# Kernel tuning notes

Hardware: AMD Instinct MI355X
Metric: run time of the kernel (lower is better)

The kernel has to match this reference:

```python
import jax, jax.numpy as jnp
import numpy as np

NUM_HEADS = 16
MAX_SEQ_LEN = 4096

def _rope_tables(head_dim, seq_len, dtype):
    inv_freq = 1.0 / (10000.0 ** (jnp.arange(0, head_dim, 2, dtype=jnp.float32) / head_dim))
    pos = jnp.arange(seq_len, dtype=jnp.float32)
    freqs = pos[:, None] * inv_freq[None, :]  # [S, hd/2]
    return jnp.cos(freqs).astype(dtype), jnp.sin(freqs).astype(dtype)

def _apply_rope(x, cos, sin):
    # x: [B, S, H, hd], interleaved even/odd pairs
    B, S, H, hd = x.shape
    xr = x.reshape(B, S, H, hd // 2, 2)
    xe, xo = xr[..., 0], xr[..., 1]
    c = cos[None, :, None, :]
    s = sin[None, :, None, :]
    ye = xe * c - xo * s
    yo = xe * s + xo * c
    return jnp.stack((ye, yo), axis=-1).reshape(B, S, H, hd)

def setup_inputs() -> dict:
    key = jax.random.key(0)
    k1, k2, k3 = jax.random.split(key, 3)
    B, S, D = 2, 2048, 2048
    x = jax.random.normal(k1, (B, S, D), dtype=jnp.float32)
    Wqkv = jax.random.normal(k2, (D, 3 * D), dtype=jnp.float32) * (D ** -0.5)
    Wo = jax.random.normal(k3, (D, D), dtype=jnp.float32) * (D ** -0.5)
    return {"x": x, "Wqkv": Wqkv, "Wo": Wo}

def reference(x, Wqkv, Wo):
    B, S, D = x.shape
    H = NUM_HEADS
    hd = D // H
    qkv = jnp.einsum('bsd,de->bse', x, Wqkv)  # [B,S,3D]
    q, k, v = jnp.split(qkv, 3, axis=-1)
    q = q.reshape(B, S, H, hd)
    k = k.reshape(B, S, H, hd)
    v = v.reshape(B, S, H, hd)
    cos, sin = _rope_tables(hd, S, x.dtype)
    q = _apply_rope(q, cos, sin)
    k = _apply_rope(k, cos, sin)
    scale = 1.0 / jnp.sqrt(jnp.asarray(hd, dtype=x.dtype))
    scores = jnp.einsum('bqhd,bkhd->bhqk', q, k) * scale  # [B,H,S,S]
    causal = jnp.tril(jnp.ones((S, S), dtype=bool))
    scores = jnp.where(causal[None, None], scores, jnp.asarray(-jnp.inf, dtype=scores.dtype))
    probs = jax.nn.softmax(scores, axis=-1)
    attn = jnp.einsum('bhqk,bkhd->bqhd', probs, v).reshape(B, S, D)
    return jnp.einsum('bsd,de->bse', attn, Wo)
```

## Files before the change

kernel.cpp:

```cpp
#include <hip/hip_runtime.h>
#include <cstddef>
#include <cstdint>
#include <math.h>

#define NB 2
#define NS 2048
#define ND 2048
#define NH 16
#define HD 128

typedef __attribute__((ext_vector_type(8))) short short8v;
typedef __attribute__((ext_vector_type(4))) float float4v;

#define MFMA16(A, B, C) __builtin_amdgcn_mfma_f32_16x16x32_bf16(A, B, C, 0, 0, 0)

__device__ __forceinline__ void split_bf16(float x, short& hi, short& lo) {
  unsigned u = __float_as_uint(x);
  unsigned hb = (u + 0x7FFFu + ((u >> 16) & 1u)) >> 16;
  float hif = __uint_as_float(hb << 16);
  float r = x - hif;
  unsigned ul = __float_as_uint(r);
  hi = (short)hb;
  lo = (short)((ul + 0x7FFFu + ((ul >> 16) & 1u)) >> 16);
}

__device__ __forceinline__ int pack2(short a, short b) {
  return (int)(unsigned short)a | ((int)(unsigned short)b << 16);
}

__global__ __launch_bounds__(256) void rope_table_kernel(float2* tab) {
  const int id = blockIdx.x * 256 + threadIdx.x;
  const int spos = id >> 6, p = id & 63;
  const float invf = powf(10000.f, -(float)p * (1.f / 64.f));
  float s, c;
  sincosf((float)spos * invf, &s, &c);
  tab[id] = make_float2(c, s);
}

__global__ __launch_bounds__(256) void transpose_split_kernel(
    const float* __restrict__ W, short* __restrict__ Th, short* __restrict__ Tl,
    int K, int N) {
  __shared__ float T[32][33];
  const int tid = threadIdx.x;
  const int n0 = blockIdx.x * 32, k0 = blockIdx.y * 32;
  {
    const int r = tid >> 3, c4 = (tid & 7) << 2;
    float4 v = *(const float4*)&W[(size_t)(k0 + r) * N + n0 + c4];
    T[r][c4 + 0] = v.x;
    T[r][c4 + 1] = v.y;
    T[r][c4 + 2] = v.z;
    T[r][c4 + 3] = v.w;
  }
  __syncthreads();
  const int n = tid >> 3, k4 = (tid & 7) << 2;
  short h[4], l[4];
#pragma unroll
  for (int e = 0; e < 4; ++e) split_bf16(T[k4 + e][n], h[e], l[e]);
  const size_t off = (size_t)(n0 + n) * K + k0 + k4;
  *(int2*)&Th[off] = make_int2(pack2(h[0], h[1]), pack2(h[2], h[3]));
  *(int2*)&Tl[off] = make_int2(pack2(l[0], l[1]), pack2(l[2], l[3]));
}

template <bool ROPE>
__global__ __launch_bounds__(256) void gemm_bf16x3_kernel(
    const float* __restrict__ A, const short* __restrict__ BTh,
    const short* __restrict__ BTl, float* __restrict__ C, int M, int N, int K,
    const float2* __restrict__ rope_tab) {
  __shared__ short Ah[128][40], Al[128][40];
  __shared__ short Bh[128][40], Bl[128][40];
  const int tid = threadIdx.x;
  const int wave = tid >> 6, lane = tid & 63;
  const int g = lane >> 4, r = lane & 15;
  const int wy = wave >> 1, wx = wave & 1;
  const int m0 = blockIdx.y * 128, n0 = blockIdx.x * 128;
  const int wm = wy * 64, wn = wx * 64;

  const int ar = tid >> 1, ac = (tid & 1) << 4;
  const int br = tid >> 1, bc = (tid & 1) << 4;

  const float* aptr = A + (size_t)(m0 + ar) * K + ac;
  const short* bhp = BTh + (size_t)(n0 + br) * K + bc;
  const short* blp = BTl + (size_t)(n0 + br) * K + bc;

  float4v acc[4][4];
#pragma unroll
  for (int i = 0; i < 4; ++i)
#pragma unroll
    for (int j = 0; j < 4; ++j) acc[i][j] = (float4v){0.f, 0.f, 0.f, 0.f};

  float4 a0 = *(const float4*)(aptr);
  float4 a1 = *(const float4*)(aptr + 4);
  float4 a2 = *(const float4*)(aptr + 8);
  float4 a3 = *(const float4*)(aptr + 12);
  int4 bh0 = *(const int4*)(bhp);
  int4 bh1 = *(const int4*)(bhp + 8);
  int4 bl0 = *(const int4*)(blp);
  int4 bl1 = *(const int4*)(blp + 8);

  for (int k0 = 0; k0 < K; k0 += 32) {
    __syncthreads();
    {
      float xs[16] = {a0.x, a0.y, a0.z, a0.w, a1.x, a1.y, a1.z, a1.w,
                      a2.x, a2.y, a2.z, a2.w, a3.x, a3.y, a3.z, a3.w};
      short h[16], l[16];
#pragma unroll
      for (int e = 0; e < 16; ++e) split_bf16(xs[e], h[e], l[e]);
      *(int4*)&Ah[ar][ac] =
          make_int4(pack2(h[0], h[1]), pack2(h[2], h[3]), pack2(h[4], h[5]),
                    pack2(h[6], h[7]));
      *(int4*)&Ah[ar][ac + 8] =
          make_int4(pack2(h[8], h[9]), pack2(h[10], h[11]),
                    pack2(h[12], h[13]), pack2(h[14], h[15]));
      *(int4*)&Al[ar][ac] =
          make_int4(pack2(l[0], l[1]), pack2(l[2], l[3]), pack2(l[4], l[5]),
                    pack2(l[6], l[7]));
      *(int4*)&Al[ar][ac + 8] =
          make_int4(pack2(l[8], l[9]), pack2(l[10], l[11]),
                    pack2(l[12], l[13]), pack2(l[14], l[15]));
      *(int4*)&Bh[br][bc] = bh0;
      *(int4*)&Bh[br][bc + 8] = bh1;
      *(int4*)&Bl[br][bc] = bl0;
      *(int4*)&Bl[br][bc + 8] = bl1;
    }
    __syncthreads();
    if (k0 + 32 < K) {
      const float* an = aptr + k0 + 32;
      a0 = *(const float4*)(an);
      a1 = *(const float4*)(an + 4);
      a2 = *(const float4*)(an + 8);
      a3 = *(const float4*)(an + 12);
      bh0 = *(const int4*)(bhp + k0 + 32);
      bh1 = *(const int4*)(bhp + k0 + 40);
      bl0 = *(const int4*)(blp + k0 + 32);
      bl1 = *(const int4*)(blp + k0 + 40);
    }
    short8v afh[4], afl[4], bfh[4], bfl[4];
#pragma unroll
    for (int mi = 0; mi < 4; ++mi) {
      afh[mi] = *(const short8v*)&Ah[wm + mi * 16 + r][8 * g];
      afl[mi] = *(const short8v*)&Al[wm + mi * 16 + r][8 * g];
    }
#pragma unroll
    for (int nj = 0; nj < 4; ++nj) {
      bfh[nj] = *(const short8v*)&Bh[wn + nj * 16 + r][8 * g];
      bfl[nj] = *(const short8v*)&Bl[wn + nj * 16 + r][8 * g];
    }
#pragma unroll
    for (int mi = 0; mi < 4; ++mi)
#pragma unroll
      for (int nj = 0; nj < 4; ++nj) {
        acc[mi][nj] = MFMA16(afh[mi], bfh[nj], acc[mi][nj]);
        acc[mi][nj] = MFMA16(afh[mi], bfl[nj], acc[mi][nj]);
        acc[mi][nj] = MFMA16(afl[mi], bfh[nj], acc[mi][nj]);
      }
  }

  if (ROPE && n0 < 2 * ND) {
    int p[4];
#pragma unroll
    for (int nj = 0; nj < 4; ++nj)
      p[nj] = ((n0 + wn + nj * 16 + r) & (HD - 1)) >> 1;
    const bool even = (r & 1) == 0;
#pragma unroll
    for (int mi = 0; mi < 4; ++mi)
#pragma unroll
      for (int j = 0; j < 4; ++j) {
        const int spos = (m0 + wm + mi * 16 + 4 * g + j) & (NS - 1);
#pragma unroll
        for (int nj = 0; nj < 4; ++nj) {
          const float2 cs = rope_tab[spos * 64 + p[nj]];
          const float own = acc[mi][nj][j];
          const float oth = __shfl_xor(own, 1);
          acc[mi][nj][j] = even ? own * cs.x - oth * cs.y
                                : oth * cs.y + own * cs.x;
        }
      }
  }
#pragma unroll
  for (int mi = 0; mi < 4; ++mi)
#pragma unroll
    for (int j = 0; j < 4; ++j) {
      const size_t row = m0 + wm + mi * 16 + 4 * g + j;
      float* Crow = C + row * N + n0 + wn;
#pragma unroll
      for (int nj = 0; nj < 4; ++nj) Crow[nj * 16 + r] = acc[mi][nj][j];
    }
}

template <bool ROPE>
__global__ __launch_bounds__(256) void gemm_f32_kernel(
    const float* __restrict__ A, const float* __restrict__ Bm,
    float* __restrict__ C, int M, int N, int K) {
  __shared__ float As[16][132];
  __shared__ float Bs[16][132];
  const int tid = threadIdx.x;
  const int m0 = blockIdx.y * 128;
  const int n0 = blockIdx.x * 128;
  const int tr = tid >> 4;
  const int tc = tid & 15;
  const int la_r = tid >> 1;
  const int la_c = (tid & 1) << 3;
  const int lb_r = tid >> 4;
  const int lb_c = (tid & 15) << 3;

  const float* Aptr = A + (size_t)(m0 + la_r) * K + la_c;
  const float* Bptr = Bm + (size_t)lb_r * N + n0 + lb_c;

  float acc[8][8] = {};

  float4 av0 = *(const float4*)(Aptr);
  float4 av1 = *(const float4*)(Aptr + 4);
  float4 bv0 = *(const float4*)(Bptr);
  float4 bv1 = *(const float4*)(Bptr + 4);

  for (int k0 = 0; k0 < K; k0 += 16) {
    __syncthreads();
    As[la_c + 0][la_r] = av0.x;
    As[la_c + 1][la_r] = av0.y;
    As[la_c + 2][la_r] = av0.z;
    As[la_c + 3][la_r] = av0.w;
    As[la_c + 4][la_r] = av1.x;
    As[la_c + 5][la_r] = av1.y;
    As[la_c + 6][la_r] = av1.z;
    As[la_c + 7][la_r] = av1.w;
    *(float4*)&Bs[lb_r][lb_c] = bv0;
    *(float4*)&Bs[lb_r][lb_c + 4] = bv1;
    __syncthreads();
    if (k0 + 16 < K) {
      const float* An = Aptr + k0 + 16;
      const float* Bn = Bptr + (size_t)(k0 + 16) * N;
      av0 = *(const float4*)(An);
      av1 = *(const float4*)(An + 4);
      bv0 = *(const float4*)(Bn);
      bv1 = *(const float4*)(Bn + 4);
    }
#pragma unroll
    for (int kk = 0; kk < 16; ++kk) {
      float a[8], b[8];
      *(float4*)&a[0] = *(const float4*)&As[kk][tr << 2];
      *(float4*)&a[4] = *(const float4*)&As[kk][64 + (tr << 2)];
      *(float4*)&b[0] = *(const float4*)&Bs[kk][tc << 2];
      *(float4*)&b[4] = *(const float4*)&Bs[kk][64 + (tc << 2)];
#pragma unroll
      for (int i = 0; i < 8; ++i)
#pragma unroll
        for (int j = 0; j < 8; ++j) acc[i][j] = fmaf(a[i], b[j], acc[i][j]);
    }
  }

  if (ROPE) {
    if ((n0 >> 11) < 2) {
#pragma unroll
      for (int g = 0; g < 2; ++g) {
        const int col = n0 + g * 64 + (tc << 2);
        const int d0 = col & (HD - 1);
        const int p0 = d0 >> 1;
        const float invf0 = powf(10000.f, -(float)p0 * (1.f / 64.f));
        const float invf1 = powf(10000.f, -(float)(p0 + 1) * (1.f / 64.f));
#pragma unroll
        for (int rg = 0; rg < 2; ++rg) {
#pragma unroll
          for (int i = 0; i < 4; ++i) {
            const int row = m0 + rg * 64 + (tr << 2) + i;
            const int spos = row & (NS - 1);
            float s0, c0, s1, c1;
            sincosf((float)spos * invf0, &s0, &c0);
            sincosf((float)spos * invf1, &s1, &c1);
            float* ar2 = &acc[rg * 4 + i][g * 4];
            const float xe0 = ar2[0], xo0 = ar2[1];
            const float xe1 = ar2[2], xo1 = ar2[3];
            ar2[0] = xe0 * c0 - xo0 * s0;
            ar2[1] = xe0 * s0 + xo0 * c0;
            ar2[2] = xe1 * c1 - xo1 * s1;
            ar2[3] = xe1 * s1 + xo1 * c1;
          }
        }
      }
    }
  }
#pragma unroll
  for (int rg = 0; rg < 2; ++rg) {
#pragma unroll
    for (int i = 0; i < 4; ++i) {
      const size_t row = m0 + rg * 64 + (tr << 2) + i;
      float* Crow = C + row * N + n0;
      float4 v0 = make_float4(acc[rg * 4 + i][0], acc[rg * 4 + i][1],
                              acc[rg * 4 + i][2], acc[rg * 4 + i][3]);
      float4 v1 = make_float4(acc[rg * 4 + i][4], acc[rg * 4 + i][5],
                              acc[rg * 4 + i][6], acc[rg * 4 + i][7]);
      *(float4*)(Crow + (tc << 2)) = v0;
      *(float4*)(Crow + 64 + (tc << 2)) = v1;
    }
  }
}

__global__ __launch_bounds__(512) void flash_attn_mfma(
    const float* __restrict__ qkv, float* __restrict__ O) {
  __shared__ short Khi[32][136];
  __shared__ short Klo[32][136];
  __shared__ short Vthi[128][40];
  __shared__ short Vtlo[128][40];
  __shared__ short Phi[8][16][40];
  __shared__ short Plo[8][16][40];

  const int tid = threadIdx.x;
  const int lane = tid & 63;
  const int wave = tid >> 6;
  const int g = lane >> 4;
  const int r = lane & 15;
  const int qtile = 15 - blockIdx.x;
  const int bh = blockIdx.y;
  const int b = bh >> 4, h = bh & 15;
  const int qb = qtile << 7;
  const int qw = qb + (wave << 4);
  const size_t row3d = 3 * ND;
  const float* base = qkv + (size_t)b * NS * row3d + (size_t)h * HD;
  const float* Kg = base + ND;
  const float* Vg = base + 2 * ND;

  const float scale = 0.088388347648318447f;
  const float* Qrow = base + (size_t)(qw + r) * row3d;
  short8v qhi[4], qlo[4];
#pragma unroll
  for (int hf = 0; hf < 4; ++hf) {
    const float* p = Qrow + 32 * hf + 8 * g;
    float4 x0 = *(const float4*)(p);
    float4 x1 = *(const float4*)(p + 4);
    float xs[8] = {x0.x, x0.y, x0.z, x0.w, x1.x, x1.y, x1.z, x1.w};
#pragma unroll
    for (int i = 0; i < 8; ++i) {
      short hi_, lo_;
      split_bf16(xs[i] * scale, hi_, lo_);
      qhi[hf][i] = hi_;
      qlo[hf][i] = lo_;
    }
  }

  float4v acc[8];
#pragma unroll
  for (int i = 0; i < 8; ++i) acc[i] = (float4v){0.f, 0.f, 0.f, 0.f};
  float m_run = -INFINITY;
  float l_run = 0.f;

  const int skv = tid >> 4;
  const int shd = (tid & 15) << 3;
  const int vkv = (tid & 15) << 1;
  const int vhd = (tid >> 4) << 2;
  const int ntiles = (qtile + 1) << 2;

  for (int t = 0; t < ntiles; ++t) {
    const int kvb = t << 5;
    __syncthreads();
    {
      const float* kr = Kg + (size_t)(kvb + skv) * row3d + shd;
#pragma unroll
      for (int u = 0; u < 2; ++u) {
        float4 v = *(const float4*)(kr + 4 * u);
        short h0, l0, h1, l1, h2, l2, h3, l3;
        split_bf16(v.x, h0, l0);
        split_bf16(v.y, h1, l1);
        split_bf16(v.z, h2, l2);
        split_bf16(v.w, h3, l3);
        *(int2*)&Khi[skv][shd + 4 * u] =
            make_int2(pack2(h0, h1), pack2(h2, h3));
        *(int2*)&Klo[skv][shd + 4 * u] =
            make_int2(pack2(l0, l1), pack2(l2, l3));
      }
    }
    {
      const float* v0p = Vg + (size_t)(kvb + vkv) * row3d + vhd;
      const float* v1p = v0p + row3d;
      float4 a0 = *(const float4*)(v0p);
      float4 b0 = *(const float4*)(v1p);
      float e0[4] = {a0.x, a0.y, a0.z, a0.w};
      float e1[4] = {b0.x, b0.y, b0.z, b0.w};
#pragma unroll
      for (int e = 0; e < 4; ++e) {
        short h0, l0, h1, l1;
        split_bf16(e0[e], h0, l0);
        split_bf16(e1[e], h1, l1);
        *(int*)&Vthi[vhd + e][vkv] = pack2(h0, h1);
        *(int*)&Vtlo[vhd + e][vkv] = pack2(l0, l1);
      }
    }
    __syncthreads();

    if (kvb <= qw + 15) {
      float4v s4[2];
#pragma unroll
      for (int f = 0; f < 2; ++f) s4[f] = (float4v){0.f, 0.f, 0.f, 0.f};
#pragma unroll
      for (int f = 0; f < 2; ++f) {
#pragma unroll
        for (int hf = 0; hf < 4; ++hf) {
          short8v ka = *(const short8v*)&Khi[16 * f + r][32 * hf + 8 * g];
          short8v kb = *(const short8v*)&Klo[16 * f + r][32 * hf + 8 * g];
          s4[f] = MFMA16(ka, qhi[hf], s4[f]);
          s4[f] = MFMA16(ka, qlo[hf], s4[f]);
          s4[f] = MFMA16(kb, qhi[hf], s4[f]);
        }
      }
      const int qglob = qw + r;
      if (kvb + 31 > qw) {
#pragma unroll
        for (int f = 0; f < 2; ++f)
#pragma unroll
          for (int j = 0; j < 4; ++j)
            if (kvb + 16 * f + 4 * g + j > qglob) s4[f][j] = -INFINITY;
      }
      float tmax = s4[0][0];
#pragma unroll
      for (int f = 0; f < 2; ++f)
#pragma unroll
        for (int j = 0; j < 4; ++j) tmax = fmaxf(tmax, s4[f][j]);
      tmax = fmaxf(tmax, __shfl_xor(tmax, 16));
      tmax = fmaxf(tmax, __shfl_xor(tmax, 32));
      const float mnew = fmaxf(m_run, tmax);
      const float alpha = __expf(m_run - mnew);
      float psum = 0.f;
      short ph[8], pl[8];
#pragma unroll
      for (int f = 0; f < 2; ++f)
#pragma unroll
        for (int j = 0; j < 4; ++j) {
          float p = __expf(s4[f][j] - mnew);
          psum += p;
          split_bf16(p, ph[4 * f + j], pl[4 * f + j]);
        }
      psum += __shfl_xor(psum, 16);
      psum += __shfl_xor(psum, 32);
      l_run = l_run * alpha + psum;
      m_run = mnew;
#pragma unroll
      for (int f = 0; f < 2; ++f) {
        *(int2*)&Phi[wave][r][16 * f + 4 * g] = make_int2(
            pack2(ph[4 * f + 0], ph[4 * f + 1]),
            pack2(ph[4 * f + 2], ph[4 * f + 3]));
        *(int2*)&Plo[wave][r][16 * f + 4 * g] = make_int2(
            pack2(pl[4 * f + 0], pl[4 * f + 1]),
            pack2(pl[4 * f + 2], pl[4 * f + 3]));
      }
      float aj[4];
#pragma unroll
      for (int j = 0; j < 4; ++j) aj[j] = __shfl(alpha, 4 * g + j);
#pragma unroll
      for (int hf = 0; hf < 8; ++hf)
#pragma unroll
        for (int j = 0; j < 4; ++j) acc[hf][j] *= aj[j];
      short8v pa = *(const short8v*)&Phi[wave][r][8 * g];
      short8v pb = *(const short8v*)&Plo[wave][r][8 * g];
#pragma unroll
      for (int hf = 0; hf < 8; ++hf) {
        short8v va = *(const short8v*)&Vthi[16 * hf + r][8 * g];
        short8v vb = *(const short8v*)&Vtlo[16 * hf + r][8 * g];
        acc[hf] = MFMA16(pa, va, acc[hf]);
        acc[hf] = MFMA16(pa, vb, acc[hf]);
        acc[hf] = MFMA16(pb, va, acc[hf]);
      }
    }
  }
  const float il = 1.f / l_run;
  float lj[4];
#pragma unroll
  for (int j = 0; j < 4; ++j) lj[j] = __shfl(il, 4 * g + j);
  float* Ob = O + ((size_t)b * NS + qw) * ND + h * HD;
#pragma unroll
  for (int hf = 0; hf < 8; ++hf)
#pragma unroll
    for (int j = 0; j < 4; ++j)
      Ob[(size_t)(4 * g + j) * ND + 16 * hf + r] = acc[hf][j] * lj[j];
}

extern "C" void kernel_launch(void* const* d_in, const int* in_sizes, int n_in,
                              void* d_out, int out_size, void* d_ws,
                              size_t ws_size, hipStream_t stream) {
  const float* x = (const float*)d_in[0];
  const float* Wqkv = (const float*)d_in[1];
  const float* Wo = (const float*)d_in[2];
  float* out = (float*)d_out;
  float* qkv = (float*)d_ws;
  float* attn = qkv + (size_t)NB * NS * 3 * ND;
  short* wqh = (short*)(attn + (size_t)NB * NS * ND);
  short* wql = wqh + (size_t)ND * 3 * ND;
  short* woh = wql + (size_t)ND * 3 * ND;
  short* wol = woh + (size_t)ND * ND;
  float2* tab = (float2*)(wol + (size_t)ND * ND);

  const size_t needed =
      ((size_t)NB * NS * 3 * ND + (size_t)NB * NS * ND) * 4 +
      ((size_t)ND * 3 * ND + (size_t)ND * ND) * 2 * 2 + (size_t)NS * 64 * 8;

  if (ws_size >= needed) {
    rope_table_kernel<<<NS * 64 / 256, 256, 0, stream>>>(tab);
    transpose_split_kernel<<<dim3(3 * ND / 32, ND / 32), 256, 0, stream>>>(
        Wqkv, wqh, wql, ND, 3 * ND);
    transpose_split_kernel<<<dim3(ND / 32, ND / 32), 256, 0, stream>>>(
        Wo, woh, wol, ND, ND);
    gemm_bf16x3_kernel<true>
        <<<dim3(3 * ND / 128, NB * NS / 128), 256, 0, stream>>>(
            x, wqh, wql, qkv, NB * NS, 3 * ND, ND, tab);
    flash_attn_mfma<<<dim3(16, 32), 512, 0, stream>>>(qkv, attn);
    gemm_bf16x3_kernel<false>
        <<<dim3(ND / 128, NB * NS / 128), 256, 0, stream>>>(
            attn, woh, wol, out, NB * NS, ND, ND, tab);
  } else {
    gemm_f32_kernel<true>
        <<<dim3(3 * ND / 128, NB * NS / 128), 256, 0, stream>>>(
            x, Wqkv, qkv, NB * NS, 3 * ND, ND);
    flash_attn_mfma<<<dim3(16, 32), 512, 0, stream>>>(qkv, attn);
    gemm_f32_kernel<false>
        <<<dim3(ND / 128, NB * NS / 128), 256, 0, stream>>>(
            attn, Wo, out, NB * NS, ND, ND);
  }
}
```

Before: 757.3 us.

## Pre-split activations to bf16 hi/lo and remap GEMM blocks per XCD

Adds a standalone kernel that splits x and the attention output into bf16 hi/lo arrays once. The GEMM then loads pre-split A tiles instead of redoing the split in every N-block. The GEMM also remaps block indices so each XCD works on a contiguous rectangular chunk of tiles, aiming for better L2 reuse. This costs two extra elementwise passes and more workspace, with a fallback to the old path when the workspace is too small.

```diff
diff --git a/kernel.cpp b/kernel.cpp
--- a/kernel.cpp
+++ b/kernel.cpp
@@ -35,6 +35,22 @@
   float s, c;
   sincosf((float)spos * invf, &s, &c);
   tab[id] = make_float2(c, s);
+}
+
+__global__ __launch_bounds__(256) void split_kernel(
+    const float* __restrict__ in, short* __restrict__ hi,
+    short* __restrict__ lo, int n4) {
+  for (int i = blockIdx.x * 256 + threadIdx.x; i < n4;
+       i += gridDim.x * 256) {
+    float4 v = ((const float4*)in)[i];
+    short h0, l0, h1, l1, h2, l2, h3, l3;
+    split_bf16(v.x, h0, l0);
+    split_bf16(v.y, h1, l1);
+    split_bf16(v.z, h2, l2);
+    split_bf16(v.w, h3, l3);
+    ((int2*)hi)[i] = make_int2(pack2(h0, h1), pack2(h2, h3));
+    ((int2*)lo)[i] = make_int2(pack2(l0, l1), pack2(l2, l3));
+  }
 }
 
 __global__ __launch_bounds__(256) void transpose_split_kernel(
@@ -61,9 +77,10 @@
   *(int2*)&Tl[off] = make_int2(pack2(l[0], l[1]), pack2(l[2], l[3]));
 }
 
-template <bool ROPE>
+template <bool ROPE, bool ASPLIT, int CHX, int CHY>
 __global__ __launch_bounds__(256) void gemm_bf16x3_kernel(
-    const float* __restrict__ A, const short* __restrict__ BTh,
+    const float* __restrict__ Af, const short* __restrict__ Ahg,
+    const short* __restrict__ Alg, const short* __restrict__ BTh,
     const short* __restrict__ BTl, float* __restrict__ C, int M, int N, int K,
     const float2* __restrict__ rope_tab) {
   __shared__ short Ah[128][40], Al[128][40];
@@ -72,15 +89,21 @@
   const int wave = tid >> 6, lane = tid & 63;
   const int g = lane >> 4, r = lane & 15;
   const int wy = wave >> 1, wx = wave & 1;
-  const int m0 = blockIdx.y * 128, n0 = blockIdx.x * 128;
+
+  int bx = blockIdx.x, by = blockIdx.y;
+  if (CHX > 0) {
+    const int flat = by * gridDim.x + bx;
+    const int xcd = flat & 7, idx = flat >> 3;
+    bx = (xcd & 3) * CHX + idx % CHX;
+    by = (xcd >> 2) * CHY + idx / CHX;
+  }
+  const int m0 = by * 128, n0 = bx * 128;
   const int wm = wy * 64, wn = wx * 64;
 
   const int ar = tid >> 1, ac = (tid & 1) << 4;
-  const int br = tid >> 1, bc = (tid & 1) << 4;
-
-  const float* aptr = A + (size_t)(m0 + ar) * K + ac;
-  const short* bhp = BTh + (size_t)(n0 + br) * K + bc;
-  const short* blp = BTl + (size_t)(n0 + br) * K + bc;
+
+  const short* bhp = BTh + (size_t)(n0 + ar) * K + ac;
+  const short* blp = BTl + (size_t)(n0 + ar) * K + ac;
 
   float4v acc[4][4];
 #pragma unroll
@@ -88,10 +111,25 @@
 #pragma unroll
     for (int j = 0; j < 4; ++j) acc[i][j] = (float4v){0.f, 0.f, 0.f, 0.f};
 
-  float4 a0 = *(const float4*)(aptr);
-  float4 a1 = *(const float4*)(aptr + 4);
-  float4 a2 = *(const float4*)(aptr + 8);
-  float4 a3 = *(const float4*)(aptr + 12);
+  float4 a0, a1, a2, a3;
+  int4 ah0, ah1, al0, al1;
+  const float* aptr = nullptr;
+  const short* ahp = nullptr;
+  const short* alp = nullptr;
+  if (ASPLIT) {
+    ahp = Ahg + (size_t)(m0 + ar) * K + ac;
+    alp = Alg + (size_t)(m0 + ar) * K + ac;
+    ah0 = *(const int4*)(ahp);
+    ah1 = *(const int4*)(ahp + 8);
+    al0 = *(const int4*)(alp);
+    al1 = *(const int4*)(alp + 8);
+  } else {
+    aptr = Af + (size_t)(m0 + ar) * K + ac;
+    a0 = *(const float4*)(aptr);
+    a1 = *(const float4*)(aptr + 4);
+    a2 = *(const float4*)(aptr + 8);
+    a3 = *(const float4*)(aptr + 12);
+  }
   int4 bh0 = *(const int4*)(bhp);
   int4 bh1 = *(const int4*)(bhp + 8);
   int4 bl0 = *(const int4*)(blp);
@@ -99,7 +137,12 @@
 
   for (int k0 = 0; k0 < K; k0 += 32) {
     __syncthreads();
-    {
+    if (ASPLIT) {
+      *(int4*)&Ah[ar][ac] = ah0;
+      *(int4*)&Ah[ar][ac + 8] = ah1;
+      *(int4*)&Al[ar][ac] = al0;
+      *(int4*)&Al[ar][ac + 8] = al1;
+    } else {
       float xs[16] = {a0.x, a0.y, a0.z, a0.w, a1.x, a1.y, a1.z, a1.w,
                       a2.x, a2.y, a2.z, a2.w, a3.x, a3.y, a3.z, a3.w};
       short h[16], l[16];
@@ -117,18 +160,25 @@
       *(int4*)&Al[ar][ac + 8] =
           make_int4(pack2(l[8], l[9]), pack2(l[10], l[11]),
                     pack2(l[12], l[13]), pack2(l[14], l[15]));
-      *(int4*)&Bh[br][bc] = bh0;
-      *(int4*)&Bh[br][bc + 8] = bh1;
-      *(int4*)&Bl[br][bc] = bl0;
-      *(int4*)&Bl[br][bc + 8] = bl1;
-    }
+    }
+    *(int4*)&Bh[ar][ac] = bh0;
+    *(int4*)&Bh[ar][ac + 8] = bh1;
+    *(int4*)&Bl[ar][ac] = bl0;
+    *(int4*)&Bl[ar][ac + 8] = bl1;
     __syncthreads();
     if (k0 + 32 < K) {
-      const float* an = aptr + k0 + 32;
-      a0 = *(const float4*)(an);
-      a1 = *(const float4*)(an + 4);
-      a2 = *(const float4*)(an + 8);
-      a3 = *(const float4*)(an + 12);
+      if (ASPLIT) {
+        ah0 = *(const int4*)(ahp + k0 + 32);
+        ah1 = *(const int4*)(ahp + k0 + 40);
+        al0 = *(const int4*)(alp + k0 + 32);
+        al1 = *(const int4*)(alp + k0 + 40);
+      } else {
+        const float* an = aptr + k0 + 32;
+        a0 = *(const float4*)(an);
+        a1 = *(const float4*)(an + 4);
+        a2 = *(const float4*)(an + 8);
+        a3 = *(const float4*)(an + 12);
+      }
       bh0 = *(const int4*)(bhp + k0 + 32);
       bh1 = *(const int4*)(bhp + k0 + 40);
       bl0 = *(const int4*)(blp + k0 + 32);
@@ -485,31 +535,49 @@
   short* woh = wql + (size_t)ND * 3 * ND;
   short* wol = woh + (size_t)ND * ND;
   float2* tab = (float2*)(wol + (size_t)ND * ND);
-
-  const size_t needed =
+  short* xh = (short*)(tab + (size_t)NS * 64);
+  short* xl = xh + (size_t)NB * NS * ND;
+  short* ath = xl + (size_t)NB * NS * ND;
+  short* atl = ath + (size_t)NB * NS * ND;
+
+  const size_t base_need =
       ((size_t)NB * NS * 3 * ND + (size_t)NB * NS * ND) * 4 +
       ((size_t)ND * 3 * ND + (size_t)ND * ND) * 2 * 2 + (size_t)NS * 64 * 8;
-
-  if (ws_size >= needed) {
+  const size_t full_need = base_need + (size_t)NB * NS * ND * 2 * 4;
+
+  const int M = NB * NS;
+  if (ws_size >= base_need) {
     rope_table_kernel<<<NS * 64 / 256, 256, 0, stream>>>(tab);
     transpose_split_kernel<<<dim3(3 * ND / 32, ND / 32), 256, 0, stream>>>(
         Wqkv, wqh, wql, ND, 3 * ND);
     transpose_split_kernel<<<dim3(ND / 32, ND / 32), 256, 0, stream>>>(
         Wo, woh, wol, ND, ND);
-    gemm_bf16x3_kernel<true>
-        <<<dim3(3 * ND / 128, NB * NS / 128), 256, 0, stream>>>(
-            x, wqh, wql, qkv, NB * NS, 3 * ND, ND, tab);
-    flash_attn_mfma<<<dim3(16, 32), 512, 0, stream>>>(qkv, attn);
-    gemm_bf16x3_kernel<false>
-        <<<dim3(ND / 128, NB * NS / 128), 256, 0, stream>>>(
-            attn, woh, wol, out, NB * NS, ND, ND, tab);
+    if (ws_size >= full_need) {
+      split_kernel<<<2048, 256, 0, stream>>>(x, xh, xl, M * ND / 4);
+      gemm_bf16x3_kernel<true, true, 12, 16>
+          <<<dim3(3 * ND / 128, M / 128), 256, 0, stream>>>(
+              nullptr, xh, xl, wqh, wql, qkv, M, 3 * ND, ND, tab);
+      flash_attn_mfma<<<dim3(16, 32), 512, 0, stream>>>(qkv, attn);
+      split_kernel<<<2048, 256, 0, stream>>>(attn, ath, atl, M * ND / 4);
+      gemm_bf16x3_kernel<false, true, 4, 16>
+          <<<dim3(ND / 128, M / 128), 256, 0, stream>>>(
+              nullptr, ath, atl, woh, wol, out, M, ND, ND, tab);
+    } else {
+      gemm_bf16x3_kernel<true, false, 0, 0>
+          <<<dim3(3 * ND / 128, M / 128), 256, 0, stream>>>(
+              x, nullptr, nullptr, wqh, wql, qkv, M, 3 * ND, ND, tab);
+      flash_attn_mfma<<<dim3(16, 32), 512, 0, stream>>>(qkv, attn);
+      gemm_bf16x3_kernel<false, false, 0, 0>
+          <<<dim3(ND / 128, M / 128), 256, 0, stream>>>(
+              attn, nullptr, nullptr, woh, wol, out, M, ND, ND, tab);
+    }
   } else {
     gemm_f32_kernel<true>
-        <<<dim3(3 * ND / 128, NB * NS / 128), 256, 0, stream>>>(
-            x, Wqkv, qkv, NB * NS, 3 * ND, ND);
+        <<<dim3(3 * ND / 128, M / 128), 256, 0, stream>>>(
+            x, Wqkv, qkv, M, 3 * ND, ND);
     flash_attn_mfma<<<dim3(16, 32), 512, 0, stream>>>(qkv, attn);
     gemm_f32_kernel<false>
-        <<<dim3(ND / 128, NB * NS / 128), 256, 0, stream>>>(
-            attn, Wo, out, NB * NS, ND, ND);
-  }
-}
+        <<<dim3(ND / 128, M / 128), 256, 0, stream>>>(
+            attn, Wo, out, M, ND, ND);
+  }
+}
```

New measurement: 754.7 us. Within noise of the previous version (-0.3%).
